# Kernel optimization log

Hardware: AMD Instinct MI355X
Metric: run time of the kernel (lower is better)

The kernel has to match this reference:

```python
import jax, jax.numpy as jnp
import numpy as np

N_NODES = 100000
N_EDGES = 600000
HIDDEN = 128


def setup_inputs() -> dict:
    key = jax.random.key(0)
    ks = jax.random.split(key, 5)
    x = jax.random.normal(ks[0], (N_NODES, HIDDEN), dtype=jnp.float32)
    edge_index = jax.random.randint(ks[1], (2, N_EDGES), 0, N_NODES, dtype=jnp.int64)
    edge_weight = jax.random.uniform(ks[2], (N_EDGES,), dtype=jnp.float32)
    # MLP params: Linear(2*H+1 -> H), ReLU, Linear(H -> 1)
    W1 = jax.random.normal(ks[3], (2 * HIDDEN + 1, HIDDEN), dtype=jnp.float32) * (1.0 / np.sqrt(2 * HIDDEN + 1))
    b1 = jnp.zeros((HIDDEN,), dtype=jnp.float32)
    W2 = jax.random.normal(ks[4], (HIDDEN, 1), dtype=jnp.float32) * (1.0 / np.sqrt(HIDDEN))
    b2 = jnp.zeros((1,), dtype=jnp.float32)
    return {"x": x, "edge_index": edge_index, "edge_weight": edge_weight,
            "W1": W1, "b1": b1, "W2": W2, "b2": b2}


def reference(x, edge_index, edge_weight, W1, b1, W2, b2):
    num_nodes = x.shape[0]
    src = edge_index[0]
    tgt = edge_index[1]
    h_src = x[src]                      # [E, H] gather
    h_tgt = x[tgt]                      # [E, H] gather
    w = edge_weight[:, None]            # [E, 1]
    concat = jnp.concatenate([h_src, h_tgt, w], axis=-1)   # [E, 2H+1]
    hidden = jax.nn.relu(concat @ W1 + b1)                 # [E, H]
    scores = (hidden @ W2 + b2)[:, 0]                      # [E]
    # NOTE: the original _softmax_edge's max-pass uses index_put_(accumulate=True)
    # on a -inf buffer, so every touched entry stays -inf and is then replaced by 0;
    # the net effect is NO max subtraction. Faithful math: plain exp / segment_sum.
    exp_scores = jnp.exp(scores)
    sum_exp = jax.ops.segment_sum(exp_scores, tgt, num_segments=num_nodes)
    sum_exp = jnp.maximum(sum_exp, 1e-12)
    alpha = exp_scores / sum_exp[tgt]                      # [E]
    out = jax.ops.segment_sum(alpha[:, None] * h_src, tgt, num_segments=num_nodes)
    return x + out
```

## Files before the change

### kernel.cpp

```cpp
#include <hip/hip_runtime.h>
#include <hip/hip_bf16.h>

#define N_NODES 100000
#define N_EDGES 600000
#define HID 128
#define SCAN_NB ((N_NODES + 255) / 256)


typedef short bf16x8 __attribute__((ext_vector_type(8)));
typedef float f32x4  __attribute__((ext_vector_type(4)));

__device__ inline unsigned short f2bf(float v) {
    __hip_bfloat16 h = __float2bfloat16(v);
    return *(unsigned short*)&h;
}
__device__ inline float bf2f(unsigned short s) {
    unsigned int u = (unsigned int)s << 16;
    return __uint_as_float(u);
}
__device__ inline float2 bfpair(unsigned int u) {
    float lo = __uint_as_float(u << 16);
    float hi = __uint_as_float(u & 0xffff0000u);
    return make_float2(lo, hi);
}

__global__ __launch_bounds__(256) void k_prep(const float* __restrict__ W1,
                                              unsigned short* __restrict__ Bh,
                                              unsigned short* __restrict__ Bl,
                                              int* __restrict__ deg)
{
    int idx = blockIdx.x * 256 + threadIdx.x;
    if (idx < N_NODES) deg[idx] = 0;
    if (idx < 32768) {
        int n = idx & 255;
        int k = idx >> 8;
        float v = (n < HID) ? W1[k * HID + n] : W1[(HID + k) * HID + (n - HID)];
        unsigned short h = f2bf(v);
        float r = v - bf2f(h);
        unsigned short l = f2bf(r);
        int dst = (k >> 5) * 8192 + n * 32 + (k & 31);
        Bh[dst] = h;
        Bl[dst] = l;
    }
}

__global__ __launch_bounds__(256) void k_gemm(const float* __restrict__ x,
                                              const unsigned short* __restrict__ BhG,
                                              const unsigned short* __restrict__ BlG,
                                              unsigned short* __restrict__ zbuf,
                                              unsigned short* __restrict__ y2buf)
{
    __shared__ unsigned short Ah[64 * 32];
    __shared__ unsigned short Al[64 * 32];

    const int tid  = threadIdx.x;
    const int bm   = blockIdx.x * 64;
    const int wave = tid >> 6;
    const int lane = tid & 63;
    const int q    = lane >> 4;
    const int ln   = lane & 15;

    const int rowA = tid >> 3;
    const int rowB = rowA + 32;
    const int f4   = tid & 7;
    const int gmA  = bm + rowA;
    const int gmB  = bm + rowB;
    const bool okA = gmA < N_NODES;
    const bool okB = gmB < N_NODES;
    const float* pxA = &x[(size_t)gmA * HID + f4 * 4];
    const float* pxB = &x[(size_t)gmB * HID + f4 * 4];

    f32x4 acc[4][4] = {};

    float4 vA = make_float4(0.f,0.f,0.f,0.f), vB = vA;
    float4 vAn = vA, vBn = vA;
    if (okA) vA = *(const float4*)pxA;
    if (okB) vB = *(const float4*)pxB;

    for (int ks = 0; ks < 4; ++ks) {
        const int k0 = ks * 32;
        {
            float4 v = vA;
            unsigned short h0 = f2bf(v.x), h1 = f2bf(v.y), h2 = f2bf(v.z), h3 = f2bf(v.w);
            unsigned int ph0 = (unsigned int)h0 | ((unsigned int)h1 << 16);
            unsigned int ph1 = (unsigned int)h2 | ((unsigned int)h3 << 16);
            unsigned short l0 = f2bf(v.x - bf2f(h0)), l1 = f2bf(v.y - bf2f(h1));
            unsigned short l2 = f2bf(v.z - bf2f(h2)), l3 = f2bf(v.w - bf2f(h3));
            unsigned int pl0 = (unsigned int)l0 | ((unsigned int)l1 << 16);
            unsigned int pl1 = (unsigned int)l2 | ((unsigned int)l3 << 16);
            int o = rowA * 32 + f4 * 4;
            *(uint2*)&Ah[o] = make_uint2(ph0, ph1);
            *(uint2*)&Al[o] = make_uint2(pl0, pl1);
            if (okA) *(uint2*)&zbuf[(size_t)gmA * 256 + 128 + k0 + f4 * 4] = make_uint2(ph0, ph1);
        }
        {
            float4 v = vB;
            unsigned short h0 = f2bf(v.x), h1 = f2bf(v.y), h2 = f2bf(v.z), h3 = f2bf(v.w);
            unsigned int ph0 = (unsigned int)h0 | ((unsigned int)h1 << 16);
            unsigned int ph1 = (unsigned int)h2 | ((unsigned int)h3 << 16);
            unsigned short l0 = f2bf(v.x - bf2f(h0)), l1 = f2bf(v.y - bf2f(h1));
            unsigned short l2 = f2bf(v.z - bf2f(h2)), l3 = f2bf(v.w - bf2f(h3));
            unsigned int pl0 = (unsigned int)l0 | ((unsigned int)l1 << 16);
            unsigned int pl1 = (unsigned int)l2 | ((unsigned int)l3 << 16);
            int o = rowB * 32 + f4 * 4;
            *(uint2*)&Ah[o] = make_uint2(ph0, ph1);
            *(uint2*)&Al[o] = make_uint2(pl0, pl1);
            if (okB) *(uint2*)&zbuf[(size_t)gmB * 256 + 128 + k0 + f4 * 4] = make_uint2(ph0, ph1);
        }
        __syncthreads();

        if (ks < 3) {
            vAn = okA ? *(const float4*)(pxA + (ks + 1) * 32) : make_float4(0.f,0.f,0.f,0.f);
            vBn = okB ? *(const float4*)(pxB + (ks + 1) * 32) : make_float4(0.f,0.f,0.f,0.f);
        }

        bf16x8 ah[4], al[4], bh[4], bl[4];
        #pragma unroll
        for (int mt = 0; mt < 4; ++mt) {
            int o = (mt * 16 + ln) * 32 + q * 8;
            ah[mt] = *(const bf16x8*)&Ah[o];
            al[mt] = *(const bf16x8*)&Al[o];
        }
        #pragma unroll
        for (int nt = 0; nt < 4; ++nt) {
            int o = ks * 8192 + (wave * 64 + nt * 16 + ln) * 32 + q * 8;
            bh[nt] = *(const bf16x8*)&BhG[o];
            bl[nt] = *(const bf16x8*)&BlG[o];
        }
        #pragma unroll
        for (int mt = 0; mt < 4; ++mt) {
            #pragma unroll
            for (int nt = 0; nt < 4; ++nt) {
                acc[mt][nt] = __builtin_amdgcn_mfma_f32_16x16x32_bf16(ah[mt], bh[nt], acc[mt][nt], 0, 0, 0);
                acc[mt][nt] = __builtin_amdgcn_mfma_f32_16x16x32_bf16(ah[mt], bl[nt], acc[mt][nt], 0, 0, 0);
                acc[mt][nt] = __builtin_amdgcn_mfma_f32_16x16x32_bf16(al[mt], bh[nt], acc[mt][nt], 0, 0, 0);
            }
        }
        __syncthreads();
        vA = vAn; vB = vBn;
    }

    #pragma unroll
    for (int mt = 0; mt < 4; ++mt) {
        #pragma unroll
        for (int r = 0; r < 4; ++r) {
            int row = bm + mt * 16 + q * 4 + r;
            if (row < N_NODES) {
                #pragma unroll
                for (int nt = 0; nt < 4; ++nt) {
                    int col = wave * 64 + nt * 16 + ln;
                    unsigned short v = f2bf(acc[mt][nt][r]);
                    if (col < 128) zbuf[(size_t)row * 256 + col] = v;
                    else           y2buf[(size_t)row * 128 + (col - 128)] = v;
                }
            }
        }
    }
}

__global__ __launch_bounds__(256) void k_count(const int* __restrict__ ei,
                                               int* __restrict__ deg)
{
    int e = blockIdx.x * blockDim.x + threadIdx.x;
    if (e < N_EDGES) atomicAdd(&deg[ei[N_EDGES + e]], 1);
}

__global__ __launch_bounds__(256) void k_partial(const int* __restrict__ deg,
                                                 int* __restrict__ partial)
{
    __shared__ int s[256];
    int t = threadIdx.x;
    int idx = blockIdx.x * 256 + t;
    s[t] = (idx < N_NODES) ? deg[idx] : 0;
    __syncthreads();
    #pragma unroll
    for (int off = 128; off > 0; off >>= 1) {
        if (t < off) s[t] += s[t + off];
        __syncthreads();
    }
    if (t == 0) partial[blockIdx.x] = s[0];
}

__global__ __launch_bounds__(512) void k_scanp(const int* __restrict__ partial,
                                               int* __restrict__ pbase)
{
    __shared__ int s[512];
    int t = threadIdx.x;
    int v = (t < SCAN_NB) ? partial[t] : 0;
    s[t] = v;
    __syncthreads();
    #pragma unroll
    for (int off = 1; off < 512; off <<= 1) {
        int u = (t >= off) ? s[t - off] : 0;
        __syncthreads();
        s[t] += u;
        __syncthreads();
    }
    if (t < SCAN_NB) pbase[t] = s[t] - v;
}

__global__ __launch_bounds__(256) void k_rowptr(const int* __restrict__ deg,
                                                const int* __restrict__ pbase,
                                                int* __restrict__ rowptr,
                                                int* __restrict__ cursor)
{
    __shared__ int s[256];
    int t = threadIdx.x;
    int b = blockIdx.x;
    int idx = b * 256 + t;
    int v = (idx < N_NODES) ? deg[idx] : 0;
    s[t] = v;
    __syncthreads();
    #pragma unroll
    for (int off = 1; off < 256; off <<= 1) {
        int u = (t >= off) ? s[t - off] : 0;
        __syncthreads();
        s[t] += u;
        __syncthreads();
    }
    if (idx < N_NODES) {
        int r = pbase[b] + s[t] - v;
        rowptr[idx] = r;
        cursor[idx] = r;
    }
    if (idx == 0) rowptr[N_NODES] = N_EDGES;
}

__global__ __launch_bounds__(256) void k_fill(const int* __restrict__ ei,
                                              const float* __restrict__ ew,
                                              int* __restrict__ cursor,
                                              uint2* __restrict__ eprs)
{
    int e = blockIdx.x * blockDim.x + threadIdx.x;
    if (e >= N_EDGES) return;
    int tgt = ei[N_EDGES + e];
    int pos = atomicAdd(&cursor[tgt], 1);
    eprs[pos] = make_uint2((unsigned int)ei[e], __float_as_uint(ew[e]));
}

__global__ __launch_bounds__(256) void k_fused(const unsigned int* __restrict__ zu,
                                               const unsigned int* __restrict__ y2u,
                                               const int* __restrict__ rowptr,
                                               const uint2* __restrict__ eprs,
                                               const float* __restrict__ x,
                                               const float* __restrict__ W1,
                                               const float* __restrict__ b1,
                                               const float* __restrict__ W2,
                                               const float* __restrict__ b2,
                                               float* __restrict__ out)
{
    int n = (blockIdx.x * blockDim.x + threadIdx.x) >> 6;
    int lane = threadIdx.x & 63;
    if (n >= N_NODES) return;
    int sl = lane & 31;
    int hl = lane >> 5;
    int c0 = sl * 4;

    uint2 uy2 = *(const uint2*)&y2u[(size_t)n * 64 + sl * 2];
    float2 y2a = bfpair(uy2.x), y2b = bfpair(uy2.y);
    float4 bv = *(const float4*)&b1[c0];
    float4 wr = *(const float4*)&W1[256 * HID + c0];
    float4 w2 = *(const float4*)&W2[c0];
    float pc0 = y2a.x + bv.x, pc1 = y2a.y + bv.y;
    float pc2 = y2b.x + bv.z, pc3 = y2b.y + bv.w;
    float b2v = b2[0];

    int beg = rowptr[n], end = rowptr[n + 1];
    float acc0 = 0.f, acc1 = 0.f, acc2 = 0.f, acc3 = 0.f, denom = 0.f;

    for (int i = beg; i < end; i += 4) {
        int idxA = i + hl;
        int idxB = i + 2 + hl;
        bool vA = idxA < end;
        bool vB = idxB < end;
        int iA = vA ? idxA : (end - 1);
        int iB = vB ? idxB : (end - 1);
        uint2 epA = eprs[iA];
        uint2 epB = eprs[iB];
        size_t bA = (size_t)epA.x * 128;
        size_t bB = (size_t)epB.x * 128;
        float wA = __uint_as_float(epA.y);
        float wB = __uint_as_float(epB.y);
        uint2 uyA = *(const uint2*)&zu[bA + sl * 2];
        uint2 uxA = *(const uint2*)&zu[bA + 64 + sl * 2];
        uint2 uyB = *(const uint2*)&zu[bB + sl * 2];
        uint2 uxB = *(const uint2*)&zu[bB + 64 + sl * 2];

        float2 aA0 = bfpair(uyA.x), aA1 = bfpair(uyA.y);
        float hA0 = fmaxf(fmaf(wA, wr.x, aA0.x + pc0), 0.f);
        float hA1 = fmaxf(fmaf(wA, wr.y, aA0.y + pc1), 0.f);
        float hA2 = fmaxf(fmaf(wA, wr.z, aA1.x + pc2), 0.f);
        float hA3 = fmaxf(fmaf(wA, wr.w, aA1.y + pc3), 0.f);
        float pA = hA0 * w2.x + hA1 * w2.y + hA2 * w2.z + hA3 * w2.w;

        float2 aB0 = bfpair(uyB.x), aB1 = bfpair(uyB.y);
        float hB0 = fmaxf(fmaf(wB, wr.x, aB0.x + pc0), 0.f);
        float hB1 = fmaxf(fmaf(wB, wr.y, aB0.y + pc1), 0.f);
        float hB2 = fmaxf(fmaf(wB, wr.z, aB1.x + pc2), 0.f);
        float hB3 = fmaxf(fmaf(wB, wr.w, aB1.y + pc3), 0.f);
        float pB = hB0 * w2.x + hB1 * w2.y + hB2 * w2.z + hB3 * w2.w;

        #pragma unroll
        for (int m = 1; m <= 16; m <<= 1) {
            pA += __shfl_xor(pA, m, 64);
            pB += __shfl_xor(pB, m, 64);
        }
        float esA = __expf(pA + b2v); if (!vA) esA = 0.f;
        float esB = __expf(pB + b2v); if (!vB) esB = 0.f;

        float2 xA0 = bfpair(uxA.x), xA1 = bfpair(uxA.y);
        float2 xB0 = bfpair(uxB.x), xB1 = bfpair(uxB.y);
        acc0 = fmaf(esA, xA0.x, acc0); acc0 = fmaf(esB, xB0.x, acc0);
        acc1 = fmaf(esA, xA0.y, acc1); acc1 = fmaf(esB, xB0.y, acc1);
        acc2 = fmaf(esA, xA1.x, acc2); acc2 = fmaf(esB, xB1.x, acc2);
        acc3 = fmaf(esA, xA1.y, acc3); acc3 = fmaf(esB, xB1.y, acc3);
        denom += esA + esB;
    }

    acc0 += __shfl_xor(acc0, 32, 64);
    acc1 += __shfl_xor(acc1, 32, 64);
    acc2 += __shfl_xor(acc2, 32, 64);
    acc3 += __shfl_xor(acc3, 32, 64);
    denom += __shfl_xor(denom, 32, 64);

    if (hl == 0) {
        float4 xt = *(const float4*)&x[(size_t)n * HID + c0];
        float inv = 1.0f / fmaxf(denom, 1e-12f);
        float4 o;
        o.x = xt.x + acc0 * inv;
        o.y = xt.y + acc1 * inv;
        o.z = xt.z + acc2 * inv;
        o.w = xt.w + acc3 * inv;
        *(float4*)&out[(size_t)n * HID + c0] = o;
    }
}

extern "C" void kernel_launch(void* const* d_in, const int* in_sizes, int n_in,
                              void* d_out, int out_size, void* d_ws, size_t ws_size,
                              hipStream_t stream) {
    const float* x  = (const float*)d_in[0];
    const int*   ei = (const int*)d_in[1];
    const float* ew = (const float*)d_in[2];
    const float* W1 = (const float*)d_in[3];
    const float* b1 = (const float*)d_in[4];
    const float* W2 = (const float*)d_in[5];
    const float* b2 = (const float*)d_in[6];
    float* out = (float*)d_out;
    char* ws = (char*)d_ws;

    const size_t deg_b    = 400000;
    const size_t rowptr_b = 400016;
    const size_t cursor_b = 400000;
    const size_t eprs_b   = 4800000;
    const size_t part_b   = 1568;
    const size_t pb_b     = 1568;
    const size_t Bh_b     = 65536;
    const size_t Bl_b     = 65536;

    char* p = ws;
    int* deg      = (int*)p;             p += deg_b;
    int* rowptr   = (int*)p;             p += rowptr_b;
    int* cursor   = (int*)p;             p += cursor_b;
    uint2* eprs   = (uint2*)p;           p += eprs_b;
    int* partial  = (int*)p;             p += part_b;
    int* pbase    = (int*)p;             p += pb_b;
    unsigned short* BhG = (unsigned short*)p;  p += Bh_b;
    unsigned short* BlG = (unsigned short*)p;  p += Bl_b;
    unsigned short* zbuf  = (unsigned short*)p;  p += (size_t)N_NODES * 256 * 2;
    unsigned short* y2buf = (unsigned short*)p;

    const int edge_blocks = (N_EDGES + 255) / 256;
    const int node_wave_blocks = (N_NODES * 64 + 255) / 256;
    const int gemm_blocks = (N_NODES + 63) / 64;

    hipLaunchKernelGGL(k_prep, dim3(SCAN_NB), dim3(256), 0, stream, W1, BhG, BlG, deg);
    hipLaunchKernelGGL(k_count, dim3(edge_blocks), dim3(256), 0, stream, ei, deg);
    hipLaunchKernelGGL(k_partial, dim3(SCAN_NB), dim3(256), 0, stream, deg, partial);
    hipLaunchKernelGGL(k_scanp, dim3(1), dim3(512), 0, stream, partial, pbase);
    hipLaunchKernelGGL(k_rowptr, dim3(SCAN_NB), dim3(256), 0, stream, deg, pbase, rowptr, cursor);
    hipLaunchKernelGGL(k_fill, dim3(edge_blocks), dim3(256), 0, stream, ei, ew, cursor, eprs);
    hipLaunchKernelGGL(k_gemm, dim3(gemm_blocks), dim3(256), 0, stream, x, BhG, BlG, zbuf, y2buf);
    hipLaunchKernelGGL(k_fused, dim3(node_wave_blocks), dim3(256), 0, stream,
                       (const unsigned int*)zbuf, (const unsigned int*)y2buf,
                       rowptr, eprs, x, W1, b1, W2, b2, out);
}
```

Before: 288.4 us.

## Drop split-bf16 GEMM correction terms and process four edges per wave

The node GEMM now uses a single bf16 product instead of the three-MFMA hi/lo split, removing the low-part weight buffer, the low-part shared tile and two thirds of the MFMAs. Separately, the fused edge kernel is remapped so each wave handles four edges per iteration with 16 lanes per edge and 8 features per lane, using 16-byte loads and a shorter shuffle reduction. The GEMM change lowers numerical accuracy of the projected features, which feed the exp scores. The GEMM part is small next to the gather-bound fused kernel.

```diff
diff --git a/kernel.cpp b/kernel.cpp
--- a/kernel.cpp
+++ b/kernel.cpp
@@ -26,7 +26,6 @@
 
 __global__ __launch_bounds__(256) void k_prep(const float* __restrict__ W1,
                                               unsigned short* __restrict__ Bh,
-                                              unsigned short* __restrict__ Bl,
                                               int* __restrict__ deg)
 {
     int idx = blockIdx.x * 256 + threadIdx.x;
@@ -35,23 +34,17 @@
         int n = idx & 255;
         int k = idx >> 8;
         float v = (n < HID) ? W1[k * HID + n] : W1[(HID + k) * HID + (n - HID)];
-        unsigned short h = f2bf(v);
-        float r = v - bf2f(h);
-        unsigned short l = f2bf(r);
         int dst = (k >> 5) * 8192 + n * 32 + (k & 31);
-        Bh[dst] = h;
-        Bl[dst] = l;
+        Bh[dst] = f2bf(v);
     }
 }
 
 __global__ __launch_bounds__(256) void k_gemm(const float* __restrict__ x,
                                               const unsigned short* __restrict__ BhG,
-                                              const unsigned short* __restrict__ BlG,
                                               unsigned short* __restrict__ zbuf,
                                               unsigned short* __restrict__ y2buf)
 {
     __shared__ unsigned short Ah[64 * 32];
-    __shared__ unsigned short Al[64 * 32];
 
     const int tid  = threadIdx.x;
     const int bm   = blockIdx.x * 64;
@@ -81,30 +74,16 @@
         const int k0 = ks * 32;
         {
             float4 v = vA;
-            unsigned short h0 = f2bf(v.x), h1 = f2bf(v.y), h2 = f2bf(v.z), h3 = f2bf(v.w);
-            unsigned int ph0 = (unsigned int)h0 | ((unsigned int)h1 << 16);
-            unsigned int ph1 = (unsigned int)h2 | ((unsigned int)h3 << 16);
-            unsigned short l0 = f2bf(v.x - bf2f(h0)), l1 = f2bf(v.y - bf2f(h1));
-            unsigned short l2 = f2bf(v.z - bf2f(h2)), l3 = f2bf(v.w - bf2f(h3));
-            unsigned int pl0 = (unsigned int)l0 | ((unsigned int)l1 << 16);
-            unsigned int pl1 = (unsigned int)l2 | ((unsigned int)l3 << 16);
-            int o = rowA * 32 + f4 * 4;
-            *(uint2*)&Ah[o] = make_uint2(ph0, ph1);
-            *(uint2*)&Al[o] = make_uint2(pl0, pl1);
+            unsigned int ph0 = (unsigned int)f2bf(v.x) | ((unsigned int)f2bf(v.y) << 16);
+            unsigned int ph1 = (unsigned int)f2bf(v.z) | ((unsigned int)f2bf(v.w) << 16);
+            *(uint2*)&Ah[rowA * 32 + f4 * 4] = make_uint2(ph0, ph1);
             if (okA) *(uint2*)&zbuf[(size_t)gmA * 256 + 128 + k0 + f4 * 4] = make_uint2(ph0, ph1);
         }
         {
             float4 v = vB;
-            unsigned short h0 = f2bf(v.x), h1 = f2bf(v.y), h2 = f2bf(v.z), h3 = f2bf(v.w);
-            unsigned int ph0 = (unsigned int)h0 | ((unsigned int)h1 << 16);
-            unsigned int ph1 = (unsigned int)h2 | ((unsigned int)h3 << 16);
-            unsigned short l0 = f2bf(v.x - bf2f(h0)), l1 = f2bf(v.y - bf2f(h1));
-            unsigned short l2 = f2bf(v.z - bf2f(h2)), l3 = f2bf(v.w - bf2f(h3));
-            unsigned int pl0 = (unsigned int)l0 | ((unsigned int)l1 << 16);
-            unsigned int pl1 = (unsigned int)l2 | ((unsigned int)l3 << 16);
-            int o = rowB * 32 + f4 * 4;
-            *(uint2*)&Ah[o] = make_uint2(ph0, ph1);
-            *(uint2*)&Al[o] = make_uint2(pl0, pl1);
+            unsigned int ph0 = (unsigned int)f2bf(v.x) | ((unsigned int)f2bf(v.y) << 16);
+            unsigned int ph1 = (unsigned int)f2bf(v.z) | ((unsigned int)f2bf(v.w) << 16);
+            *(uint2*)&Ah[rowB * 32 + f4 * 4] = make_uint2(ph0, ph1);
             if (okB) *(uint2*)&zbuf[(size_t)gmB * 256 + 128 + k0 + f4 * 4] = make_uint2(ph0, ph1);
         }
         __syncthreads();
@@ -114,26 +93,20 @@
             vBn = okB ? *(const float4*)(pxB + (ks + 1) * 32) : make_float4(0.f,0.f,0.f,0.f);
         }
 
-        bf16x8 ah[4], al[4], bh[4], bl[4];
+        bf16x8 ah[4], bh[4];
         #pragma unroll
         for (int mt = 0; mt < 4; ++mt) {
-            int o = (mt * 16 + ln) * 32 + q * 8;
-            ah[mt] = *(const bf16x8*)&Ah[o];
-            al[mt] = *(const bf16x8*)&Al[o];
+            ah[mt] = *(const bf16x8*)&Ah[(mt * 16 + ln) * 32 + q * 8];
         }
         #pragma unroll
         for (int nt = 0; nt < 4; ++nt) {
-            int o = ks * 8192 + (wave * 64 + nt * 16 + ln) * 32 + q * 8;
-            bh[nt] = *(const bf16x8*)&BhG[o];
-            bl[nt] = *(const bf16x8*)&BlG[o];
+            bh[nt] = *(const bf16x8*)&BhG[ks * 8192 + (wave * 64 + nt * 16 + ln) * 32 + q * 8];
         }
         #pragma unroll
         for (int mt = 0; mt < 4; ++mt) {
             #pragma unroll
             for (int nt = 0; nt < 4; ++nt) {
                 acc[mt][nt] = __builtin_amdgcn_mfma_f32_16x16x32_bf16(ah[mt], bh[nt], acc[mt][nt], 0, 0, 0);
-                acc[mt][nt] = __builtin_amdgcn_mfma_f32_16x16x32_bf16(ah[mt], bl[nt], acc[mt][nt], 0, 0, 0);
-                acc[mt][nt] = __builtin_amdgcn_mfma_f32_16x16x32_bf16(al[mt], bh[nt], acc[mt][nt], 0, 0, 0);
             }
         }
         __syncthreads();
@@ -252,86 +225,80 @@
     int n = (blockIdx.x * blockDim.x + threadIdx.x) >> 6;
     int lane = threadIdx.x & 63;
     if (n >= N_NODES) return;
-    int sl = lane & 31;
-    int hl = lane >> 5;
-    int c0 = sl * 4;
-
-    uint2 uy2 = *(const uint2*)&y2u[(size_t)n * 64 + sl * 2];
-    float2 y2a = bfpair(uy2.x), y2b = bfpair(uy2.y);
-    float4 bv = *(const float4*)&b1[c0];
-    float4 wr = *(const float4*)&W1[256 * HID + c0];
-    float4 w2 = *(const float4*)&W2[c0];
-    float pc0 = y2a.x + bv.x, pc1 = y2a.y + bv.y;
-    float pc2 = y2b.x + bv.z, pc3 = y2b.y + bv.w;
+    int ql = lane & 15;
+    int qi = lane >> 4;
+    int c0 = ql * 8;
+
+    uint4 uy2 = *(const uint4*)&y2u[(size_t)n * 64 + ql * 4];
+    float2 y2a = bfpair(uy2.x), y2b = bfpair(uy2.y), y2c = bfpair(uy2.z), y2d = bfpair(uy2.w);
+    float4 bv0 = *(const float4*)&b1[c0];
+    float4 bv1 = *(const float4*)&b1[c0 + 4];
+    float4 wr0 = *(const float4*)&W1[256 * HID + c0];
+    float4 wr1 = *(const float4*)&W1[256 * HID + c0 + 4];
+    float4 w20 = *(const float4*)&W2[c0];
+    float4 w21 = *(const float4*)&W2[c0 + 4];
+    float p0 = y2a.x + bv0.x, p1 = y2a.y + bv0.y, p2 = y2b.x + bv0.z, p3 = y2b.y + bv0.w;
+    float p4 = y2c.x + bv1.x, p5 = y2c.y + bv1.y, p6 = y2d.x + bv1.z, p7 = y2d.y + bv1.w;
     float b2v = b2[0];
 
     int beg = rowptr[n], end = rowptr[n + 1];
-    float acc0 = 0.f, acc1 = 0.f, acc2 = 0.f, acc3 = 0.f, denom = 0.f;
+    float a0 = 0.f, a1 = 0.f, a2 = 0.f, a3 = 0.f;
+    float a4 = 0.f, a5 = 0.f, a6 = 0.f, a7 = 0.f;
+    float denom = 0.f;
 
     for (int i = beg; i < end; i += 4) {
-        int idxA = i + hl;
-        int idxB = i + 2 + hl;
-        bool vA = idxA < end;
-        bool vB = idxB < end;
-        int iA = vA ? idxA : (end - 1);
-        int iB = vB ? idxB : (end - 1);
-        uint2 epA = eprs[iA];
-        uint2 epB = eprs[iB];
-        size_t bA = (size_t)epA.x * 128;
-        size_t bB = (size_t)epB.x * 128;
-        float wA = __uint_as_float(epA.y);
-        float wB = __uint_as_float(epB.y);
-        uint2 uyA = *(const uint2*)&zu[bA + sl * 2];
-        uint2 uxA = *(const uint2*)&zu[bA + 64 + sl * 2];
-        uint2 uyB = *(const uint2*)&zu[bB + sl * 2];
-        uint2 uxB = *(const uint2*)&zu[bB + 64 + sl * 2];
-
-        float2 aA0 = bfpair(uyA.x), aA1 = bfpair(uyA.y);
-        float hA0 = fmaxf(fmaf(wA, wr.x, aA0.x + pc0), 0.f);
-        float hA1 = fmaxf(fmaf(wA, wr.y, aA0.y + pc1), 0.f);
-        float hA2 = fmaxf(fmaf(wA, wr.z, aA1.x + pc2), 0.f);
-        float hA3 = fmaxf(fmaf(wA, wr.w, aA1.y + pc3), 0.f);
-        float pA = hA0 * w2.x + hA1 * w2.y + hA2 * w2.z + hA3 * w2.w;
-
-        float2 aB0 = bfpair(uyB.x), aB1 = bfpair(uyB.y);
-        float hB0 = fmaxf(fmaf(wB, wr.x, aB0.x + pc0), 0.f);
-        float hB1 = fmaxf(fmaf(wB, wr.y, aB0.y + pc1), 0.f);
-        float hB2 = fmaxf(fmaf(wB, wr.z, aB1.x + pc2), 0.f);
-        float hB3 = fmaxf(fmaf(wB, wr.w, aB1.y + pc3), 0.f);
-        float pB = hB0 * w2.x + hB1 * w2.y + hB2 * w2.z + hB3 * w2.w;
-
-        #pragma unroll
-        for (int m = 1; m <= 16; m <<= 1) {
-            pA += __shfl_xor(pA, m, 64);
-            pB += __shfl_xor(pB, m, 64);
-        }
-        float esA = __expf(pA + b2v); if (!vA) esA = 0.f;
-        float esB = __expf(pB + b2v); if (!vB) esB = 0.f;
-
-        float2 xA0 = bfpair(uxA.x), xA1 = bfpair(uxA.y);
-        float2 xB0 = bfpair(uxB.x), xB1 = bfpair(uxB.y);
-        acc0 = fmaf(esA, xA0.x, acc0); acc0 = fmaf(esB, xB0.x, acc0);
-        acc1 = fmaf(esA, xA0.y, acc1); acc1 = fmaf(esB, xB0.y, acc1);
-        acc2 = fmaf(esA, xA1.x, acc2); acc2 = fmaf(esB, xB1.x, acc2);
-        acc3 = fmaf(esA, xA1.y, acc3); acc3 = fmaf(esB, xB1.y, acc3);
-        denom += esA + esB;
-    }
-
-    acc0 += __shfl_xor(acc0, 32, 64);
-    acc1 += __shfl_xor(acc1, 32, 64);
-    acc2 += __shfl_xor(acc2, 32, 64);
-    acc3 += __shfl_xor(acc3, 32, 64);
-    denom += __shfl_xor(denom, 32, 64);
-
-    if (hl == 0) {
-        float4 xt = *(const float4*)&x[(size_t)n * HID + c0];
+        int idx = i + qi;
+        bool valid = idx < end;
+        int ie = valid ? idx : (end - 1);
+        uint2 ep = eprs[ie];
+        size_t base = (size_t)ep.x * 128;
+        float w = __uint_as_float(ep.y);
+        uint4 uy = *(const uint4*)&zu[base + ql * 4];
+        uint4 ux = *(const uint4*)&zu[base + 64 + ql * 4];
+
+        float2 ya = bfpair(uy.x), yb = bfpair(uy.y), yc = bfpair(uy.z), yd = bfpair(uy.w);
+        float h0 = fmaxf(fmaf(w, wr0.x, ya.x + p0), 0.f);
+        float h1 = fmaxf(fmaf(w, wr0.y, ya.y + p1), 0.f);
+        float h2 = fmaxf(fmaf(w, wr0.z, yb.x + p2), 0.f);
+        float h3 = fmaxf(fmaf(w, wr0.w, yb.y + p3), 0.f);
+        float h4 = fmaxf(fmaf(w, wr1.x, yc.x + p4), 0.f);
+        float h5 = fmaxf(fmaf(w, wr1.y, yc.y + p5), 0.f);
+        float h6 = fmaxf(fmaf(w, wr1.z, yd.x + p6), 0.f);
+        float h7 = fmaxf(fmaf(w, wr1.w, yd.y + p7), 0.f);
+        float s = ((h0 * w20.x + h1 * w20.y) + (h2 * w20.z + h3 * w20.w))
+                + ((h4 * w21.x + h5 * w21.y) + (h6 * w21.z + h7 * w21.w));
+        #pragma unroll
+        for (int m = 1; m <= 8; m <<= 1) s += __shfl_xor(s, m, 64);
+        float es = valid ? __expf(s + b2v) : 0.f;
+
+        float2 xa = bfpair(ux.x), xb = bfpair(ux.y), xc = bfpair(ux.z), xd = bfpair(ux.w);
+        a0 = fmaf(es, xa.x, a0); a1 = fmaf(es, xa.y, a1);
+        a2 = fmaf(es, xb.x, a2); a3 = fmaf(es, xb.y, a3);
+        a4 = fmaf(es, xc.x, a4); a5 = fmaf(es, xc.y, a5);
+        a6 = fmaf(es, xd.x, a6); a7 = fmaf(es, xd.y, a7);
+        denom += es;
+    }
+
+    #pragma unroll
+    for (int m = 16; m <= 32; m <<= 1) {
+        a0 += __shfl_xor(a0, m, 64); a1 += __shfl_xor(a1, m, 64);
+        a2 += __shfl_xor(a2, m, 64); a3 += __shfl_xor(a3, m, 64);
+        a4 += __shfl_xor(a4, m, 64); a5 += __shfl_xor(a5, m, 64);
+        a6 += __shfl_xor(a6, m, 64); a7 += __shfl_xor(a7, m, 64);
+        denom += __shfl_xor(denom, m, 64);
+    }
+
+    if (qi == 0) {
+        float4 xt0 = *(const float4*)&x[(size_t)n * HID + c0];
+        float4 xt1 = *(const float4*)&x[(size_t)n * HID + c0 + 4];
         float inv = 1.0f / fmaxf(denom, 1e-12f);
-        float4 o;
-        o.x = xt.x + acc0 * inv;
-        o.y = xt.y + acc1 * inv;
-        o.z = xt.z + acc2 * inv;
-        o.w = xt.w + acc3 * inv;
-        *(float4*)&out[(size_t)n * HID + c0] = o;
+        float4 o0, o1;
+        o0.x = xt0.x + a0 * inv; o0.y = xt0.y + a1 * inv;
+        o0.z = xt0.z + a2 * inv; o0.w = xt0.w + a3 * inv;
+        o1.x = xt1.x + a4 * inv; o1.y = xt1.y + a5 * inv;
+        o1.z = xt1.z + a6 * inv; o1.w = xt1.w + a7 * inv;
+        *(float4*)&out[(size_t)n * HID + c0]     = o0;
+        *(float4*)&out[(size_t)n * HID + c0 + 4] = o1;
     }
 }
 
@@ -355,7 +322,6 @@
     const size_t part_b   = 1568;
     const size_t pb_b     = 1568;
     const size_t Bh_b     = 65536;
-    const size_t Bl_b     = 65536;
 
     char* p = ws;
     int* deg      = (int*)p;             p += deg_b;
@@ -365,7 +331,6 @@
     int* partial  = (int*)p;             p += part_b;
     int* pbase    = (int*)p;             p += pb_b;
     unsigned short* BhG = (unsigned short*)p;  p += Bh_b;
-    unsigned short* BlG = (unsigned short*)p;  p += Bl_b;
     unsigned short* zbuf  = (unsigned short*)p;  p += (size_t)N_NODES * 256 * 2;
     unsigned short* y2buf = (unsigned short*)p;
 
@@ -373,13 +338,13 @@
     const int node_wave_blocks = (N_NODES * 64 + 255) / 256;
     const int gemm_blocks = (N_NODES + 63) / 64;
 
-    hipLaunchKernelGGL(k_prep, dim3(SCAN_NB), dim3(256), 0, stream, W1, BhG, BlG, deg);
+    hipLaunchKernelGGL(k_prep, dim3(SCAN_NB), dim3(256), 0, stream, W1, BhG, deg);
     hipLaunchKernelGGL(k_count, dim3(edge_blocks), dim3(256), 0, stream, ei, deg);
     hipLaunchKernelGGL(k_partial, dim3(SCAN_NB), dim3(256), 0, stream, deg, partial);
     hipLaunchKernelGGL(k_scanp, dim3(1), dim3(512), 0, stream, partial, pbase);
     hipLaunchKernelGGL(k_rowptr, dim3(SCAN_NB), dim3(256), 0, stream, deg, pbase, rowptr, cursor);
     hipLaunchKernelGGL(k_fill, dim3(edge_blocks), dim3(256), 0, stream, ei, ew, cursor, eprs);
-    hipLaunchKernelGGL(k_gemm, dim3(gemm_blocks), dim3(256), 0, stream, x, BhG, BlG, zbuf, y2buf);
+    hipLaunchKernelGGL(k_gemm, dim3(gemm_blocks), dim3(256), 0, stream, x, BhG, zbuf, y2buf);
     hipLaunchKernelGGL(k_fused, dim3(node_wave_blocks), dim3(256), 0, stream,
                        (const unsigned int*)zbuf, (const unsigned int*)y2buf,
                        rowptr, eprs, x, W1, b1, W2, b2, out);
```

After: 279.5 us. -3.1%, faster.
